# Optimization experiments

Measured on AMD Instinct MI355X. Metric: run time of the kernel, lower is better.

Reference implementation:

```python
import jax, jax.numpy as jnp
import numpy as np

H = 16      # query heads
G = 4       # kv heads
D = 64      # head dim
ROPE_BASE = 10000.0

def _rotate_half(t):
    t1, t2 = jnp.split(t, 2, axis=-1)
    return jnp.concatenate([-t2, t1], axis=-1)

def _rope_emb(n):
    inv_freq = 1.0 / (ROPE_BASE ** (jnp.arange(0, D, 2, dtype=jnp.float32) / D))
    freqs = jnp.outer(jnp.arange(n, dtype=jnp.float32), inv_freq)  # [n, D/2]
    return jnp.concatenate([freqs, freqs], axis=-1)               # [n, D]

def setup_inputs() -> dict:
    key = jax.random.key(0)
    k1, k2, k3, k4 = jax.random.split(key, 4)
    B, N, C = 2, 2048, 1024
    x = jax.random.normal(k1, (B, N, C), dtype=jnp.float32)
    w_q = jax.random.normal(k2, (C, C), dtype=jnp.float32) * 0.02
    w_kv = jax.random.normal(k3, (C, 2 * G * D), dtype=jnp.float32) * 0.02
    w_out = jax.random.normal(k4, (C, C), dtype=jnp.float32) * 0.02
    return {"x": x, "w_q": w_q, "w_kv": w_kv, "w_out": w_out}

def reference(x, w_q, w_kv, w_out):
    B, N, C = x.shape
    scale = D ** -0.5
    q = (x @ w_q).reshape(B, N, H, D).transpose(0, 2, 1, 3)        # [B,H,N,D]
    kv = x @ w_kv
    k, v = jnp.split(kv, 2, axis=-1)
    k = k.reshape(B, N, G, D).transpose(0, 2, 1, 3)                # [B,G,N,D]
    v = v.reshape(B, N, G, D).transpose(0, 2, 1, 3)
    emb = _rope_emb(N)                                             # [N,D]
    cos, sin = jnp.cos(emb), jnp.sin(emb)
    q = q * cos + _rotate_half(q) * sin
    k = k * cos + _rotate_half(k) * sin
    # NOTE: faithful to source einsum -- kv-head axis g is SUMMED (absent from output)
    scores = jnp.einsum('bhid,bgjd->bhij', q, k) * scale           # [B,H,N,N]
    probs = jax.nn.softmax(scores, axis=-1)
    out = jnp.einsum('bhij,bgjd->bhid', probs, v)                  # [B,H,N,D]
    out = out.transpose(0, 2, 1, 3).reshape(B, N, H * D)
    return out @ w_out
```

## Files before the change

### kernel.cpp

```cpp
#include <hip/hip_runtime.h>
#include <hip/hip_bf16.h>
#include <math.h>

#define B_ 2
#define N_ 2048
#define C_ 1024
#define H_ 16
#define G_ 4
#define D_ 64

using short8  = __attribute__((ext_vector_type(8))) short;
using short4v = __attribute__((ext_vector_type(4))) short;
using float4v = __attribute__((ext_vector_type(4))) float;

#if __has_builtin(__builtin_amdgcn_mfma_f32_16x16x16_bf16)
#define MFMA16K16(A, B, C) __builtin_amdgcn_mfma_f32_16x16x16_bf16(A, B, C, 0, 0, 0)
#else
#define MFMA16K16(A, B, C) __builtin_amdgcn_mfma_f32_16x16x16bf16_1k(A, B, C, 0, 0, 0)
#endif

__device__ __forceinline__ ushort f2bf(float f) {
    union { float f; unsigned u; } v; v.f = f;
    unsigned r = (v.u + 0x7FFF + ((v.u >> 16) & 1)) >> 16;
    return (ushort)r;
}
__device__ __forceinline__ float bf2f(ushort u) {
    union { unsigned u; float f; } t; t.u = ((unsigned)u) << 16; return t.f;
}
__device__ __forceinline__ unsigned pack_bf16(float a, float b) {
#if __has_builtin(__builtin_amdgcn_cvt_pk_bf16_f32)
    auto t = __builtin_amdgcn_cvt_pk_bf16_f32(a, b);
    unsigned r; __builtin_memcpy(&r, &t, 4); return r;
#else
    return (unsigned)f2bf(a) | ((unsigned)f2bf(b) << 16);
#endif
}
__device__ __forceinline__ float fexp2(float x) {
#if __has_builtin(__builtin_amdgcn_exp2f)
    return __builtin_amdgcn_exp2f(x);
#else
    return exp2f(x);
#endif
}

__global__ void convert_x(const float* __restrict__ x, ushort* __restrict__ xb) {
    int i = (blockIdx.x * 256 + threadIdx.x) * 4;
    float4 v = *(const float4*)(x + i);
    ushort4 o;
    o.x = f2bf(v.x); o.y = f2bf(v.y); o.z = f2bf(v.z); o.w = f2bf(v.w);
    *(ushort4*)(xb + i) = o;
}

__global__ void tconv(const float* __restrict__ src, ushort* __restrict__ dst,
                      int K, int N) {
    __shared__ float T[64][65];
    const int n0 = blockIdx.x * 64, k0 = blockIdx.y * 64;
    const int tid = threadIdx.x;
    #pragma unroll
    for (int s = 0; s < 16; ++s) {
        int idx = tid + s * 256; int r = idx >> 6, cc = idx & 63;
        T[r][cc] = src[(size_t)(k0 + r) * N + n0 + cc];
    }
    __syncthreads();
    #pragma unroll
    for (int s = 0; s < 16; ++s) {
        int idx = tid + s * 256; int r = idx >> 6, cc = idx & 63;
        dst[(size_t)(n0 + r) * K + k0 + cc] = f2bf(T[cc][r]);
    }
}

template <bool F32OUT>
__global__ __launch_bounds__(256) void gemm64(const ushort* __restrict__ A,
                                              const ushort* __restrict__ Bt,
                                              void* __restrict__ Cv,
                                              int M, int N, int K) {
    __shared__ __align__(16) ushort As[64 * 64];
    __shared__ __align__(16) ushort Bs[64 * 64];

    const int tid = threadIdx.x, wave = tid >> 6, lane = tid & 63;
    const int g = lane >> 4, c = lane & 15;
    const int wr = wave >> 1, wc = wave & 1;
    const int m0 = blockIdx.y * 64, n0 = blockIdx.x * 64;

    const int lr8 = lane >> 3, lq8 = lane & 7;
    const int gchunk = (lq8 ^ lr8) * 8;
    const ushort* pa = A  + (size_t)(m0 + wave * 16 + lr8) * K + gchunk;
    const ushort* pb = Bt + (size_t)(n0 + wave * 16 + lr8) * K + gchunk;

    float4v acc[2][2] = {{{0,0,0,0},{0,0,0,0}},{{0,0,0,0},{0,0,0,0}}};

    for (int k0 = 0; k0 < K; k0 += 64) {
        #pragma unroll
        for (int t = 0; t < 2; ++t) {
            __builtin_amdgcn_global_load_lds(
                (const __attribute__((address_space(1))) void*)(pa + (size_t)t * 8 * K + k0),
                (__attribute__((address_space(3))) void*)&As[(wave * 16 + t * 8) * 64], 16, 0, 0);
            __builtin_amdgcn_global_load_lds(
                (const __attribute__((address_space(1))) void*)(pb + (size_t)t * 8 * K + k0),
                (__attribute__((address_space(3))) void*)&Bs[(wave * 16 + t * 8) * 64], 16, 0, 0);
        }
        __syncthreads();

        #pragma unroll
        for (int kk = 0; kk < 2; ++kk) {
            const int c7 = c & 7;
            short8 af0 = *(const short8*)&As[(wr * 32 + c) * 64 + ((kk * 4 + g) ^ c7) * 8];
            short8 af1 = *(const short8*)&As[(wr * 32 + 16 + c) * 64 + ((kk * 4 + g) ^ c7) * 8];
            short8 bf0 = *(const short8*)&Bs[(wc * 32 + c) * 64 + ((kk * 4 + g) ^ c7) * 8];
            short8 bf1 = *(const short8*)&Bs[(wc * 32 + 16 + c) * 64 + ((kk * 4 + g) ^ c7) * 8];
            acc[0][0] = __builtin_amdgcn_mfma_f32_16x16x32_bf16(af0, bf0, acc[0][0], 0, 0, 0);
            acc[0][1] = __builtin_amdgcn_mfma_f32_16x16x32_bf16(af0, bf1, acc[0][1], 0, 0, 0);
            acc[1][0] = __builtin_amdgcn_mfma_f32_16x16x32_bf16(af1, bf0, acc[1][0], 0, 0, 0);
            acc[1][1] = __builtin_amdgcn_mfma_f32_16x16x32_bf16(af1, bf1, acc[1][1], 0, 0, 0);
        }
        __syncthreads();
    }

    #pragma unroll
    for (int a = 0; a < 2; ++a)
        #pragma unroll
        for (int bb = 0; bb < 2; ++bb)
            #pragma unroll
            for (int r = 0; r < 4; ++r) {
                int rowi = m0 + wr * 32 + a * 16 + 4 * g + r;
                int coli = n0 + wc * 32 + bb * 16 + c;
                if (F32OUT) ((float*)Cv)[(size_t)rowi * N + coli] = acc[a][bb][r];
                else ((ushort*)Cv)[(size_t)rowi * N + coli] = f2bf(acc[a][bb][r]);
            }
}

__global__ void kv_reduce2(const ushort* __restrict__ qkvb,
                           ushort* __restrict__ Kt, ushort* __restrict__ VtT) {
    const int wid = threadIdx.x >> 6, d = threadIdx.x & 63;
    const int rowg = blockIdx.x * 4 + wid;
    const int n = rowg & (N_ - 1), b = rowg >> 11;

    const ushort* base = qkvb + (size_t)rowg * 1536 + 1024;
    float ks = 0.f, vs = 0.f;
    #pragma unroll
    for (int g = 0; g < G_; ++g) {
        ks += bf2f(base[g * 64 + d]);
        vs += bf2f(base[256 + g * 64 + d]);
    }
    float partner = __shfl_xor(ks, 32, 64);
    float rh = (d < 32) ? -partner : partner;
    float ang = (float)n * __powf(10000.0f, -(float)(d & 31) * (1.0f / 32.0f));
    float sn, cs; __sincosf(ang, &sn, &cs);

    Kt[(size_t)rowg * 64 + d] = f2bf(ks * cs + rh * sn);
    VtT[((size_t)b * 64 + d) * N_ + n] = f2bf(vs);
}

#define KSV 72
#define QSCALE 0.18033688011112042f

__global__ __launch_bounds__(256) void attn8(
        const ushort* __restrict__ qkvb, const ushort* __restrict__ Kt,
        const ushort* __restrict__ VtT,
        ushort* __restrict__ oP0, ushort* __restrict__ oP1,
        float* __restrict__ lP0, float* __restrict__ lP1) {
    const int s  = blockIdx.x & 1;
    const int qt = (blockIdx.x >> 1) & 7;
    const int h  = (blockIdx.x >> 4) & 15;
    const int b  = blockIdx.x >> 8;
    const int tid = threadIdx.x, wave = tid >> 6, lane = tid & 63;
    const int g = lane >> 4, c = lane & 15;

    __shared__ __align__(16) ushort Ksh[64 * KSV];
    __shared__ __align__(16) ushort Vsh[64 * KSV];

    ushort* oPs = s ? oP1 : oP0;
    float*  lPs = s ? lP1 : lP0;

    const int i0 = qt * 256 + wave * 64;
    float invf[8];
    #pragma unroll
    for (int i = 0; i < 8; ++i)
        invf[i] = __powf(10000.0f, -(float)(8 * g + i) * (1.0f / 32.0f));

    short8 qf[4][2];
    #pragma unroll
    for (int a = 0; a < 4; ++a) {
        const int row = i0 + a * 16 + c;
        const ushort* qrow = qkvb + (size_t)(b * N_ + row) * 1536 + h * 64;
        short8 raw0 = *(const short8*)(qrow + 8 * g);
        short8 raw1 = *(const short8*)(qrow + 32 + 8 * g);
        #pragma unroll
        for (int i = 0; i < 8; ++i) {
            float f0 = bf2f((ushort)raw0[i]), f1 = bf2f((ushort)raw1[i]);
            float sn, cs; __sincosf((float)row * invf[i], &sn, &cs);
            qf[a][0][i] = (short)f2bf((f0 * cs - f1 * sn) * QSCALE);
            qf[a][1][i] = (short)f2bf((f1 * cs + f0 * sn) * QSCALE);
        }
    }

    float4v o[4][4];
    #pragma unroll
    for (int a = 0; a < 4; ++a)
        #pragma unroll
        for (int f = 0; f < 4; ++f) o[a][f] = {0, 0, 0, 0};
    float ll[4] = {0.f, 0.f, 0.f, 0.f};

    const ushort* Kb = Kt  + (size_t)b * N_ * 64;
    const ushort* Vb = VtT + (size_t)b * 64 * N_;
    const int lr8 = lane >> 3, lq8 = lane & 7;
    const int j0 = s * (N_ / 2);
    const int NT = (N_ / 2) / 64;

    short8 kr0 = *(const short8*)(Kb + (size_t)(j0 + wave * 16 + lr8) * 64 + lq8 * 8);
    short8 kr1 = *(const short8*)(Kb + (size_t)(j0 + wave * 16 + 8 + lr8) * 64 + lq8 * 8);
    short8 vr0 = *(const short8*)(Vb + (size_t)(wave * 16 + lr8) * N_ + j0 + lq8 * 8);
    short8 vr1 = *(const short8*)(Vb + (size_t)(wave * 16 + 8 + lr8) * N_ + j0 + lq8 * 8);

    for (int t = 0; t < NT; ++t) {
        __syncthreads();
        *(short8*)&Ksh[(wave * 16 + lr8) * KSV + lq8 * 8]     = kr0;
        *(short8*)&Ksh[(wave * 16 + 8 + lr8) * KSV + lq8 * 8] = kr1;
        *(short8*)&Vsh[(wave * 16 + lr8) * KSV + lq8 * 8]     = vr0;
        *(short8*)&Vsh[(wave * 16 + 8 + lr8) * KSV + lq8 * 8] = vr1;
        __syncthreads();
        if (t + 1 < NT) {
            const int jn = j0 + (t + 1) * 64;
            kr0 = *(const short8*)(Kb + (size_t)(jn + wave * 16 + lr8) * 64 + lq8 * 8);
            kr1 = *(const short8*)(Kb + (size_t)(jn + wave * 16 + 8 + lr8) * 64 + lq8 * 8);
            vr0 = *(const short8*)(Vb + (size_t)(wave * 16 + lr8) * N_ + jn + lq8 * 8);
            vr1 = *(const short8*)(Vb + (size_t)(wave * 16 + 8 + lr8) * N_ + jn + lq8 * 8);
        }

        #pragma unroll
        for (int jt4 = 0; jt4 < 4; ++jt4) {
            const int R = jt4 * 16 + c;
            short8 kf0 = *(const short8*)&Ksh[R * KSV + 8 * g];
            short8 kf1 = *(const short8*)&Ksh[R * KSV + 32 + 8 * g];
            short4v vf[4];
            #pragma unroll
            for (int f = 0; f < 4; ++f)
                vf[f] = *(const short4v*)&Vsh[(16 * f + c) * KSV + jt4 * 16 + 4 * g];

            #pragma unroll
            for (int a = 0; a < 4; ++a) {
                float4v st = {0, 0, 0, 0};
                st = __builtin_amdgcn_mfma_f32_16x16x32_bf16(kf0, qf[a][0], st, 0, 0, 0);
                st = __builtin_amdgcn_mfma_f32_16x16x32_bf16(kf1, qf[a][1], st, 0, 0, 0);
                float p0 = fexp2(st[0]), p1 = fexp2(st[1]);
                float p2 = fexp2(st[2]), p3 = fexp2(st[3]);
                ll[a] += (p0 + p1) + (p2 + p3);
                union { unsigned u[2]; short4v v; } pk;
                pk.u[0] = pack_bf16(p0, p1);
                pk.u[1] = pack_bf16(p2, p3);
                #pragma unroll
                for (int f = 0; f < 4; ++f)
                    o[a][f] = MFMA16K16(vf[f], pk.v, o[a][f]);
            }
        }
    }

    #pragma unroll
    for (int a = 0; a < 4; ++a) {
        float lt = ll[a];
        lt += __shfl_xor(lt, 16, 64);
        lt += __shfl_xor(lt, 32, 64);
        const int row = i0 + a * 16 + c;
        if (g == 0) lPs[(size_t)(b * N_ + row) * 16 + h] = lt;
        #pragma unroll
        for (int f = 0; f < 4; ++f) {
            ushort4 w;
            w.x = f2bf(o[a][f][0]); w.y = f2bf(o[a][f][1]);
            w.z = f2bf(o[a][f][2]); w.w = f2bf(o[a][f][3]);
            *(ushort4*)(oPs + (size_t)(b * N_ + row) * 1024 + h * 64 + 16 * f + 4 * g) = w;
        }
    }
}

__global__ void combine(const ushort* __restrict__ oP0, const ushort* __restrict__ oP1,
                        const float* __restrict__ lP0, const float* __restrict__ lP1,
                        ushort* __restrict__ ao) {
    const int e = (blockIdx.x * 256 + threadIdx.x) * 4;
    const int row = e >> 10, hh = (e >> 6) & 15;
    const float inv = 1.0f / (lP0[row * 16 + hh] + lP1[row * 16 + hh]);
    ushort4 a = *(const ushort4*)(oP0 + e);
    ushort4 b = *(const ushort4*)(oP1 + e);
    ushort4 r;
    r.x = f2bf((bf2f(a.x) + bf2f(b.x)) * inv);
    r.y = f2bf((bf2f(a.y) + bf2f(b.y)) * inv);
    r.z = f2bf((bf2f(a.z) + bf2f(b.z)) * inv);
    r.w = f2bf((bf2f(a.w) + bf2f(b.w)) * inv);
    *(ushort4*)(ao + e) = r;
}

extern "C" void kernel_launch(void* const* d_in, const int* in_sizes, int n_in,
                              void* d_out, int out_size, void* d_ws, size_t ws_size,
                              hipStream_t stream) {
    const float* x     = (const float*)d_in[0];
    const float* w_q   = (const float*)d_in[1];
    const float* w_kv  = (const float*)d_in[2];
    const float* w_out = (const float*)d_in[3];
    float* out = (float*)d_out;

    const int M = B_ * N_;
    ushort* xb    = (ushort*)d_ws;
    ushort* wqkvT = xb    + (size_t)M * C_;
    ushort* woutT = wqkvT + (size_t)1536 * C_;
    ushort* qkvb  = woutT + (size_t)C_ * C_;
    ushort* Kt    = qkvb  + (size_t)M * 1536;
    ushort* VtT   = Kt    + (size_t)B_ * N_ * D_;
    ushort* oP1   = VtT   + (size_t)B_ * D_ * N_;
    float*  lP0   = (float*)(oP1 + (size_t)M * C_);
    float*  lP1   = lP0 + (size_t)M * H_;
    ushort* oP0   = xb;
    ushort* ao    = xb;

    convert_x<<<(M * C_) / 1024, 256, 0, stream>>>(x, xb);
    tconv<<<dim3(16, 16), 256, 0, stream>>>(w_q,  wqkvT,                   C_, C_);
    tconv<<<dim3(8, 16),  256, 0, stream>>>(w_kv, wqkvT + (size_t)C_ * C_, C_, 2 * G_ * D_);
    tconv<<<dim3(16, 16), 256, 0, stream>>>(w_out, woutT,                  C_, C_);

    gemm64<false><<<dim3(1536 / 64, M / 64), 256, 0, stream>>>(xb, wqkvT, qkvb, M, 1536, C_);
    kv_reduce2<<<M / 4, 256, 0, stream>>>(qkvb, Kt, VtT);
    attn8<<<B_ * H_ * (N_ / 256) * 2, 256, 0, stream>>>(qkvb, Kt, VtT, oP0, oP1, lP0, lP1);
    combine<<<(M * C_) / 1024, 256, 0, stream>>>(oP0, oP1, lP0, lP1, ao);
    gemm64<true><<<dim3(C_ / 64, M / 64), 256, 0, stream>>>(ao, woutT, out, M, C_, C_);
}
```

Before: 189.9 us.

## Pre-sum KV-head weights, fuse prep kernels, and swizzle attention LDS layout

Because the reference sums the kv-head axis, the per-head K and V weight columns are summed once in the weight prep. The QKV GEMM then produces 1152 columns instead of 1536, and the post-GEMM reduction turns into plain rope and copy. The x conversion and weight transposes are merged into a single prep launch to cut launch overhead. The attention LDS tiles drop row padding in favour of XOR-swizzled offsets to avoid bank conflicts. Summing the weights in fp32 before the bf16 rounding changes the rounding slightly compared with summing bf16 outputs.

After: 182.3 us. -4.0%, faster.

```diff
diff --git a/kernel.cpp b/kernel.cpp
--- a/kernel.cpp
+++ b/kernel.cpp
@@ -8,6 +8,7 @@
 #define H_ 16
 #define G_ 4
 #define D_ 64
+#define QKV_N 1152
 
 using short8  = __attribute__((ext_vector_type(8))) short;
 using short4v = __attribute__((ext_vector_type(4))) short;
@@ -43,18 +44,9 @@
 #endif
 }
 
-__global__ void convert_x(const float* __restrict__ x, ushort* __restrict__ xb) {
-    int i = (blockIdx.x * 256 + threadIdx.x) * 4;
-    float4 v = *(const float4*)(x + i);
-    ushort4 o;
-    o.x = f2bf(v.x); o.y = f2bf(v.y); o.z = f2bf(v.z); o.w = f2bf(v.w);
-    *(ushort4*)(xb + i) = o;
-}
-
-__global__ void tconv(const float* __restrict__ src, ushort* __restrict__ dst,
-                      int K, int N) {
-    __shared__ float T[64][65];
-    const int n0 = blockIdx.x * 64, k0 = blockIdx.y * 64;
+__device__ void tconv_body(const float* __restrict__ src, ushort* __restrict__ dst,
+                           int K, int N, int bx, int by, float (*T)[65]) {
+    const int n0 = bx * 64, k0 = by * 64;
     const int tid = threadIdx.x;
     #pragma unroll
     for (int s = 0; s < 16; ++s) {
@@ -66,6 +58,47 @@
     for (int s = 0; s < 16; ++s) {
         int idx = tid + s * 256; int r = idx >> 6, cc = idx & 63;
         dst[(size_t)(n0 + r) * K + k0 + cc] = f2bf(T[cc][r]);
+    }
+}
+
+__global__ void prep(const float* __restrict__ x, const float* __restrict__ w_q,
+                     const float* __restrict__ w_kv, const float* __restrict__ w_out,
+                     ushort* __restrict__ xb, ushort* __restrict__ wqkvT,
+                     ushort* __restrict__ woutT) {
+    __shared__ float T[64][65];
+    const int blk = blockIdx.x, tid = threadIdx.x;
+    if (blk < 4096) {
+        int i = blk * 1024 + tid * 4;
+        float4 v = *(const float4*)(x + i);
+        ushort4 o;
+        o.x = f2bf(v.x); o.y = f2bf(v.y); o.z = f2bf(v.z); o.w = f2bf(v.w);
+        *(ushort4*)(xb + i) = o;
+    } else if (blk < 4352) {
+        int idx = blk - 4096;
+        tconv_body(w_q, wqkvT, C_, C_, idx & 15, idx >> 4, T);
+    } else if (blk < 4608) {
+        int idx = blk - 4352;
+        tconv_body(w_out, woutT, C_, C_, idx & 15, idx >> 4, T);
+    } else {
+        const int k0 = (blk - 4608) * 64;
+        #pragma unroll
+        for (int it = 0; it < 4; ++it) {
+            int p = tid + it * 256;
+            int kk = p >> 4, d4 = (p & 15) * 4;
+            float ks[4] = {0, 0, 0, 0}, vs[4] = {0, 0, 0, 0};
+            #pragma unroll
+            for (int g = 0; g < G_; ++g) {
+                float4 a = *(const float4*)(w_kv + (size_t)(k0 + kk) * 512 + g * 64 + d4);
+                float4 b = *(const float4*)(w_kv + (size_t)(k0 + kk) * 512 + 256 + g * 64 + d4);
+                ks[0] += a.x; ks[1] += a.y; ks[2] += a.z; ks[3] += a.w;
+                vs[0] += b.x; vs[1] += b.y; vs[2] += b.z; vs[3] += b.w;
+            }
+            #pragma unroll
+            for (int e = 0; e < 4; ++e) {
+                wqkvT[(size_t)(1024 + d4 + e) * C_ + k0 + kk] = f2bf(ks[e]);
+                wqkvT[(size_t)(1088 + d4 + e) * C_ + k0 + kk] = f2bf(vs[e]);
+            }
+        }
     }
 }
 
@@ -129,32 +162,26 @@
             }
 }
 
-__global__ void kv_reduce2(const ushort* __restrict__ qkvb,
-                           ushort* __restrict__ Kt, ushort* __restrict__ VtT) {
+__global__ void rope_kv(const ushort* __restrict__ qkvb,
+                        ushort* __restrict__ Kt, ushort* __restrict__ VtT) {
     const int wid = threadIdx.x >> 6, d = threadIdx.x & 63;
     const int rowg = blockIdx.x * 4 + wid;
     const int n = rowg & (N_ - 1), b = rowg >> 11;
 
-    const ushort* base = qkvb + (size_t)rowg * 1536 + 1024;
-    float ks = 0.f, vs = 0.f;
-    #pragma unroll
-    for (int g = 0; g < G_; ++g) {
-        ks += bf2f(base[g * 64 + d]);
-        vs += bf2f(base[256 + g * 64 + d]);
-    }
+    const ushort* base = qkvb + (size_t)rowg * QKV_N + 1024;
+    float ks = bf2f(base[d]);
     float partner = __shfl_xor(ks, 32, 64);
     float rh = (d < 32) ? -partner : partner;
     float ang = (float)n * __powf(10000.0f, -(float)(d & 31) * (1.0f / 32.0f));
     float sn, cs; __sincosf(ang, &sn, &cs);
 
     Kt[(size_t)rowg * 64 + d] = f2bf(ks * cs + rh * sn);
-    VtT[((size_t)b * 64 + d) * N_ + n] = f2bf(vs);
-}
-
-#define KSV 72
+    VtT[((size_t)b * 64 + d) * N_ + n] = base[64 + d];
+}
+
 #define QSCALE 0.18033688011112042f
 
-__global__ __launch_bounds__(256) void attn8(
+__global__ __launch_bounds__(256) void attn9(
         const ushort* __restrict__ qkvb, const ushort* __restrict__ Kt,
         const ushort* __restrict__ VtT,
         ushort* __restrict__ oP0, ushort* __restrict__ oP1,
@@ -166,8 +193,8 @@
     const int tid = threadIdx.x, wave = tid >> 6, lane = tid & 63;
     const int g = lane >> 4, c = lane & 15;
 
-    __shared__ __align__(16) ushort Ksh[64 * KSV];
-    __shared__ __align__(16) ushort Vsh[64 * KSV];
+    __shared__ __align__(16) ushort Ksh[64 * 64];
+    __shared__ __align__(16) ushort Vsh[64 * 64];
 
     ushort* oPs = s ? oP1 : oP0;
     float*  lPs = s ? lP1 : lP0;
@@ -182,7 +209,7 @@
     #pragma unroll
     for (int a = 0; a < 4; ++a) {
         const int row = i0 + a * 16 + c;
-        const ushort* qrow = qkvb + (size_t)(b * N_ + row) * 1536 + h * 64;
+        const ushort* qrow = qkvb + (size_t)(b * N_ + row) * QKV_N + h * 64;
         short8 raw0 = *(const short8*)(qrow + 8 * g);
         short8 raw1 = *(const short8*)(qrow + 32 + 8 * g);
         #pragma unroll
@@ -204,6 +231,7 @@
     const ushort* Kb = Kt  + (size_t)b * N_ * 64;
     const ushort* Vb = VtT + (size_t)b * 64 * N_;
     const int lr8 = lane >> 3, lq8 = lane & 7;
+    const int wpos = (lq8 ^ lr8) * 8;
     const int j0 = s * (N_ / 2);
     const int NT = (N_ / 2) / 64;
 
@@ -214,10 +242,10 @@
 
     for (int t = 0; t < NT; ++t) {
         __syncthreads();
-        *(short8*)&Ksh[(wave * 16 + lr8) * KSV + lq8 * 8]     = kr0;
-        *(short8*)&Ksh[(wave * 16 + 8 + lr8) * KSV + lq8 * 8] = kr1;
-        *(short8*)&Vsh[(wave * 16 + lr8) * KSV + lq8 * 8]     = vr0;
-        *(short8*)&Vsh[(wave * 16 + 8 + lr8) * KSV + lq8 * 8] = vr1;
+        *(short8*)&Ksh[(wave * 16 + lr8) * 64 + wpos]     = kr0;
+        *(short8*)&Ksh[(wave * 16 + 8 + lr8) * 64 + wpos] = kr1;
+        *(short8*)&Vsh[(wave * 16 + lr8) * 64 + wpos]     = vr0;
+        *(short8*)&Vsh[(wave * 16 + 8 + lr8) * 64 + wpos] = vr1;
         __syncthreads();
         if (t + 1 < NT) {
             const int jn = j0 + (t + 1) * 64;
@@ -230,12 +258,13 @@
         #pragma unroll
         for (int jt4 = 0; jt4 < 4; ++jt4) {
             const int R = jt4 * 16 + c;
-            short8 kf0 = *(const short8*)&Ksh[R * KSV + 8 * g];
-            short8 kf1 = *(const short8*)&Ksh[R * KSV + 32 + 8 * g];
+            short8 kf0 = *(const short8*)&Ksh[R * 64 + ((g ^ (c & 7)) * 8)];
+            short8 kf1 = *(const short8*)&Ksh[R * 64 + (((g ^ 4) ^ (c & 7)) * 8)];
             short4v vf[4];
             #pragma unroll
             for (int f = 0; f < 4; ++f)
-                vf[f] = *(const short4v*)&Vsh[(16 * f + c) * KSV + jt4 * 16 + 4 * g];
+                vf[f] = *(const short4v*)&Vsh[(16 * f + c) * 64 +
+                          (((jt4 * 2 + (g >> 1)) ^ (c & 7)) * 8) + (g & 1) * 4];
 
             #pragma unroll
             for (int a = 0; a < 4; ++a) {
@@ -300,9 +329,9 @@
     const int M = B_ * N_;
     ushort* xb    = (ushort*)d_ws;
     ushort* wqkvT = xb    + (size_t)M * C_;
-    ushort* woutT = wqkvT + (size_t)1536 * C_;
+    ushort* woutT = wqkvT + (size_t)QKV_N * C_;
     ushort* qkvb  = woutT + (size_t)C_ * C_;
-    ushort* Kt    = qkvb  + (size_t)M * 1536;
+    ushort* Kt    = qkvb  + (size_t)M * QKV_N;
     ushort* VtT   = Kt    + (size_t)B_ * N_ * D_;
     ushort* oP1   = VtT   + (size_t)B_ * D_ * N_;
     float*  lP0   = (float*)(oP1 + (size_t)M * C_);
@@ -310,14 +339,10 @@
     ushort* oP0   = xb;
     ushort* ao    = xb;
 
-    convert_x<<<(M * C_) / 1024, 256, 0, stream>>>(x, xb);
-    tconv<<<dim3(16, 16), 256, 0, stream>>>(w_q,  wqkvT,                   C_, C_);
-    tconv<<<dim3(8, 16),  256, 0, stream>>>(w_kv, wqkvT + (size_t)C_ * C_, C_, 2 * G_ * D_);
-    tconv<<<dim3(16, 16), 256, 0, stream>>>(w_out, woutT,                  C_, C_);
-
-    gemm64<false><<<dim3(1536 / 64, M / 64), 256, 0, stream>>>(xb, wqkvT, qkvb, M, 1536, C_);
-    kv_reduce2<<<M / 4, 256, 0, stream>>>(qkvb, Kt, VtT);
-    attn8<<<B_ * H_ * (N_ / 256) * 2, 256, 0, stream>>>(qkvb, Kt, VtT, oP0, oP1, lP0, lP1);
+    prep<<<4624, 256, 0, stream>>>(x, w_q, w_kv, w_out, xb, wqkvT, woutT);
+    gemm64<false><<<dim3(QKV_N / 64, M / 64), 256, 0, stream>>>(xb, wqkvT, qkvb, M, QKV_N, C_);
+    rope_kv<<<M / 4, 256, 0, stream>>>(qkvb, Kt, VtT);
+    attn9<<<B_ * H_ * (N_ / 256) * 2, 256, 0, stream>>>(qkvb, Kt, VtT, oP0, oP1, lP0, lP1);
     combine<<<(M * C_) / 1024, 256, 0, stream>>>(oP0, oP1, lP0, lP1, ao);
     gemm64<true><<<dim3(C_ / 64, M / 64), 256, 0, stream>>>(ao, woutT, out, M, C_, C_);
 }
```
